# Performance work log

Measured on AMD Instinct MI355X. Metric: run time of the kernel, lower is better.

Reference implementation:

```python
import jax, jax.numpy as jnp
import numpy as np
import math

DIM = 2048
N_HEADS = 32
N_KV_HEADS = 8
HEAD_DIM = DIM // N_HEADS  # 64
N_REP = N_HEADS // N_KV_HEADS  # 4
BSZ, SEQ = 2, 2048


def setup_inputs() -> dict:
    key = jax.random.key(0)
    ks = jax.random.split(key, 8)
    x = jax.random.normal(ks[0], (BSZ, SEQ, DIM), dtype=jnp.float32)
    # rotary tables, [seq, head_dim//2]
    inv_freq = 1.0 / (10000.0 ** (np.arange(0, HEAD_DIM, 2, dtype=np.float32) / HEAD_DIM))
    t = np.arange(SEQ, dtype=np.float32)
    freqs = np.outer(t, inv_freq)
    freqs_cos = jnp.asarray(np.cos(freqs))
    freqs_sin = jnp.asarray(np.sin(freqs))
    s = 0.02
    wq = jax.random.normal(ks[1], (DIM, N_HEADS * HEAD_DIM), dtype=jnp.float32) * s
    wk = jax.random.normal(ks[2], (DIM, N_KV_HEADS * HEAD_DIM), dtype=jnp.float32) * s
    wv = jax.random.normal(ks[3], (DIM, N_KV_HEADS * HEAD_DIM), dtype=jnp.float32) * s
    wo = jax.random.normal(ks[4], (N_HEADS * HEAD_DIM, DIM), dtype=jnp.float32) * s
    return {"x": x, "freqs_cos": freqs_cos, "freqs_sin": freqs_sin,
            "wq": wq, "wk": wk, "wv": wv, "wo": wo}


def _apply_rotary(xq, xk, cos, sin):
    # xq: [b,s,h,d], xk: [b,s,kh,d]; cos/sin: [s, d//2]
    def rot(t):
        tr = t[..., 0::2]  # even -> real
        ti = t[..., 1::2]  # odd  -> imag
        c = cos[None, :, None, :]
        s_ = sin[None, :, None, :]
        or_ = tr * c - ti * s_
        oi_ = tr * s_ + ti * c
        # interleave back: [..., d//2, 2] -> [..., d]
        return jnp.stack([or_, oi_], axis=-1).reshape(t.shape)
    return rot(xq), rot(xk)


def reference(x, freqs_cos, freqs_sin, wq, wk, wv, wo):
    b, s, _ = x.shape
    xq = (x @ wq).reshape(b, s, N_HEADS, HEAD_DIM)
    xk = (x @ wk).reshape(b, s, N_KV_HEADS, HEAD_DIM)
    xv = (x @ wv).reshape(b, s, N_KV_HEADS, HEAD_DIM)
    xq, xk = _apply_rotary(xq, xk, freqs_cos, freqs_sin)
    # repeat_kv: [b,s,kh,d] -> [b,s,kh*n_rep,d]
    xk = jnp.repeat(xk, N_REP, axis=2)
    xv = jnp.repeat(xv, N_REP, axis=2)
    # [b,h,s,d]
    q = xq.transpose(0, 2, 1, 3)
    k = xk.transpose(0, 2, 1, 3)
    v = xv.transpose(0, 2, 1, 3)
    scale = 1.0 / math.sqrt(HEAD_DIM)
    scores = jnp.einsum('bhqd,bhkd->bhqk', q, k) * scale
    causal = jnp.tril(jnp.ones((s, s), dtype=bool))
    scores = jnp.where(causal[None, None], scores, jnp.float32(-jnp.inf))
    probs = jax.nn.softmax(scores, axis=-1)
    out = jnp.einsum('bhqk,bhkd->bhqd', probs, v)  # [b,h,s,d]
    out = out.transpose(0, 2, 1, 3).reshape(b, s, N_HEADS * HEAD_DIM)
    return out @ wo
```

## Files before the change

### kernel.cpp

```cpp
#include <hip/hip_runtime.h>
#include <hip/hip_bf16.h>

typedef __attribute__((ext_vector_type(8))) short short8;
typedef __attribute__((ext_vector_type(4))) float f32x4;

__device__ __forceinline__ unsigned short f2bf(float f) {
  union { float f; unsigned u; } v; v.f = f;
  unsigned r = v.u + 0x7FFFu + ((v.u >> 16) & 1u);
  return (unsigned short)(r >> 16);
}
__device__ __forceinline__ float bf2f(unsigned short h) {
  union { unsigned u; float f; } v; v.u = ((unsigned)h) << 16;
  return v.f;
}
__device__ __forceinline__ unsigned pkbf(float a, float b) {
  __hip_bfloat162 h = __float22bfloat162_rn(float2{a, b});
  union { __hip_bfloat162 h; unsigned u; } cv; cv.h = h;
  return cv.u;
}

__global__ void prep(const float* __restrict__ x, const float* __restrict__ wq,
                     const float* __restrict__ wk, const float* __restrict__ wv,
                     const float* __restrict__ wo, unsigned short* __restrict__ xb,
                     unsigned short* __restrict__ wt, unsigned short* __restrict__ wot) {
  const int z = blockIdx.z, tid = threadIdx.x;
  if (z == 0) {
    int id = blockIdx.y * 64 + blockIdx.x;
#pragma unroll
    for (int rep = 0; rep < 2; ++rep) {
      int i = (rep * 4096 + id) * 256 + tid;
      float4 v = ((const float4*)x)[i];
      ushort4 o;
      o.x = f2bf(v.x); o.y = f2bf(v.y); o.z = f2bf(v.z); o.w = f2bf(v.w);
      ((ushort4*)xb)[i] = o;
    }
    return;
  }
  __shared__ float tile[32][33];
  const float* src;
  unsigned short* dst;
  int N;
  if (z == 1) { src = wq; dst = wt; N = 2048; }
  else if (z == 2) { src = wk; dst = wt + 2048ull * 2048; N = 512; }
  else if (z == 3) { src = wv; dst = wt + 2560ull * 2048; N = 512; }
  else { src = wo; dst = wot; N = 2048; }
  const int K = 2048;
  int n0 = blockIdx.x * 32, k0 = blockIdx.y * 32;
  if (n0 >= N) return;
  int xx = tid & 31, yy = tid >> 5;
#pragma unroll
  for (int j = 0; j < 4; ++j) tile[yy + 8 * j][xx] = src[(size_t)(k0 + yy + 8 * j) * N + n0 + xx];
  __syncthreads();
#pragma unroll
  for (int j = 0; j < 4; ++j) dst[(size_t)(n0 + yy + 8 * j) * K + k0 + xx] = f2bf(tile[xx][yy + 8 * j]);
}

template <int MODE>
__global__ __launch_bounds__(256, 2) void gemm_bt64(const unsigned short* __restrict__ A,
                                                    const unsigned short* __restrict__ Bt,
                                                    void* __restrict__ Cv, int K, int ldc,
                                                    unsigned short* __restrict__ vt) {
  __shared__ alignas(16) unsigned short As[128 * 64];
  __shared__ alignas(16) unsigned short Bs[128 * 64];
  const int t = threadIdx.x;
  const int lane = t & 63, w = t >> 6;
  const int l15 = lane & 15, quad = lane >> 4;
  const int bn0 = blockIdx.x * 128, bm0 = blockIdx.y * 128;
  const int wm = (w >> 1) * 64, wn = (w & 1) * 64;
  const unsigned short* Ab = A + (size_t)bm0 * K;
  const unsigned short* Bb = Bt + (size_t)bn0 * K;
  const int asw = l15 & 7;

  f32x4 acc[4][4];
  const f32x4 zf = {0.f, 0.f, 0.f, 0.f};
#pragma unroll
  for (int i = 0; i < 4; ++i)
#pragma unroll
    for (int j = 0; j < 4; ++j) acc[i][j] = zf;

  for (int k0 = 0; k0 < K; k0 += 64) {
    __syncthreads();
#pragma unroll
    for (int r = 0; r < 4; ++r) {
      int e = r * 256 + t;
      int row = e >> 3, cslot = e & 7;
      int cg = cslot ^ (row & 7);
      const unsigned short* ga = Ab + (size_t)row * K + k0 + cg * 8;
      __builtin_amdgcn_global_load_lds((const __attribute__((address_space(1))) void*)ga,
                                       (__attribute__((address_space(3))) void*)(As + e * 8), 16, 0, 0);
      const unsigned short* gb = Bb + (size_t)row * K + k0 + cg * 8;
      __builtin_amdgcn_global_load_lds((const __attribute__((address_space(1))) void*)gb,
                                       (__attribute__((address_space(3))) void*)(Bs + e * 8), 16, 0, 0);
    }
    __syncthreads();
#pragma unroll
    for (int s = 0; s < 2; ++s) {
      short8 af[4], bf[4];
#pragma unroll
      for (int i = 0; i < 4; ++i)
        af[i] = *reinterpret_cast<const short8*>(As + (wm + i * 16 + l15) * 64 + (((s * 4 + quad) ^ asw) * 8));
#pragma unroll
      for (int j = 0; j < 4; ++j)
        bf[j] = *reinterpret_cast<const short8*>(Bs + (wn + j * 16 + l15) * 64 + (((s * 4 + quad) ^ asw) * 8));
#pragma unroll
      for (int i = 0; i < 4; ++i)
#pragma unroll
        for (int j = 0; j < 4; ++j)
          acc[i][j] = __builtin_amdgcn_mfma_f32_16x16x32_bf16(af[i], bf[j], acc[i][j], 0, 0, 0);
    }
  }

  if (MODE == 1 && bn0 >= 2560) {
    const int b = bm0 >> 11;
#pragma unroll
    for (int i = 0; i < 4; ++i) {
      int srow = (bm0 + wm + i * 16 + quad * 4) & 2047;
#pragma unroll
      for (int j = 0; j < 4; ++j) {
        int vcol = bn0 - 2560 + wn + j * 16 + l15;
        int kvh = vcol >> 6, d = vcol & 63;
        uint2 pk = make_uint2(pkbf(acc[i][j][0], acc[i][j][1]), pkbf(acc[i][j][2], acc[i][j][3]));
        *reinterpret_cast<uint2*>(vt + ((size_t)(b * 8 + kvh) * 64 + d) * 2048 + srow) = pk;
      }
    }
  } else {
#pragma unroll
    for (int i = 0; i < 4; ++i)
#pragma unroll
      for (int j = 0; j < 4; ++j)
#pragma unroll
        for (int r = 0; r < 4; ++r) {
          size_t row = (size_t)(bm0 + wm + i * 16 + quad * 4 + r);
          size_t col = (size_t)(bn0 + wn + j * 16 + l15);
          if (MODE == 1)
            ((unsigned short*)Cv)[row * ldc + col] = f2bf(acc[i][j][r]);
          else
            ((float*)Cv)[row * ldc + col] = acc[i][j][r];
        }
  }
}

__global__ void rope_k(unsigned short* __restrict__ qkv, const float* __restrict__ fcos,
                       const float* __restrict__ fsin) {
  int tid = blockIdx.x * 256 + threadIdx.x;
  int row = tid >> 8, p = tid & 255;
  int col = 2048 + 2 * p;
  int s = row & 2047;
  int fi = p & 31;
  float c = fcos[s * 32 + fi], sn = fsin[s * 32 + fi];
  unsigned int* ptr = (unsigned int*)(qkv + (size_t)row * 2560 + col);
  unsigned int pr = *ptr;
  float xr = bf2f((unsigned short)(pr & 0xFFFFu));
  float xi = bf2f((unsigned short)(pr >> 16));
  float orr = xr * c - xi * sn;
  float oi = xr * sn + xi * c;
  *ptr = ((unsigned)f2bf(oi) << 16) | (unsigned)f2bf(orr);
}

__global__ __launch_bounds__(256, 4) void flash_attn(const unsigned short* __restrict__ qkv,
                                                     const unsigned short* __restrict__ vt,
                                                     const float* __restrict__ fcos,
                                                     const float* __restrict__ fsin,
                                                     unsigned short* __restrict__ out) {
  __shared__ alignas(16) unsigned short Ks[64 * 64];
  __shared__ alignas(16) unsigned short Vs[64 * 64];
  __shared__ alignas(16) unsigned short Ps[128 * 64];
  __shared__ float Ls[128];
  const int t = threadIdx.x, lane = t & 63, w = t >> 6;
  const int l15 = lane & 15, quad = lane >> 4;
  const int h = blockIdx.y, b = blockIdx.z;
  const int qb = ((int)blockIdx.x ^ (15 * (h >> 4))) & 15;
  const int q0 = qb * 128;
  const int kvh = h >> 2;
  const size_t rowB = (size_t)b * 2048;
  const unsigned short* Qg = qkv + (rowB + q0) * 2560 + h * 64;
  const unsigned short* Kg = qkv + rowB * 2560 + 2048 + kvh * 64;
  const unsigned short* Vtg = vt + (size_t)(b * 8 + kvh) * 64 * 2048;
  const float SC = 0.18033688011112042f;

  short8 qf[2][2];
#pragma unroll
  for (int mt = 0; mt < 2; ++mt)
#pragma unroll
    for (int s = 0; s < 2; ++s) {
      int qrow = w * 32 + mt * 16 + l15;
      short8 raw = *reinterpret_cast<const short8*>(Qg + (size_t)qrow * 2560 + s * 32 + quad * 8);
      f32x4 c4 = *reinterpret_cast<const f32x4*>(fcos + (size_t)(q0 + qrow) * 32 + s * 16 + quad * 4);
      f32x4 s4 = *reinterpret_cast<const f32x4*>(fsin + (size_t)(q0 + qrow) * 32 + s * 16 + quad * 4);
      short8 o;
#pragma unroll
      for (int k = 0; k < 4; ++k) {
        float xr = bf2f((unsigned short)raw[2 * k]);
        float xi = bf2f((unsigned short)raw[2 * k + 1]);
        o[2 * k] = (short)f2bf((xr * c4[k] - xi * s4[k]) * SC);
        o[2 * k + 1] = (short)f2bf((xr * s4[k] + xi * c4[k]) * SC);
      }
      qf[mt][s] = o;
    }

  const f32x4 zf = {0.f, 0.f, 0.f, 0.f};
  f32x4 oacc[2][4];
#pragma unroll
  for (int mt = 0; mt < 2; ++mt)
#pragma unroll
    for (int nt = 0; nt < 4; ++nt) oacc[mt][nt] = zf;
  float lsum[2] = {0.f, 0.f};

  const int kb_end = 2 * qb + 2;
  const int srow = t >> 3, sc8 = t & 7;
  const int soff = srow * 64 + ((sc8 ^ (srow & 7)) * 8);
  const int asw = l15 & 7;
  short8 kreg[2], vreg[2];
#pragma unroll
  for (int r = 0; r < 2; ++r) {
    kreg[r] = *reinterpret_cast<const short8*>(Kg + (size_t)(srow + 32 * r) * 2560 + sc8 * 8);
    vreg[r] = *reinterpret_cast<const short8*>(Vtg + (size_t)(srow + 32 * r) * 2048 + sc8 * 8);
  }

  for (int kb = 0; kb < kb_end; ++kb) {
    __syncthreads();
#pragma unroll
    for (int r = 0; r < 2; ++r) {
      *reinterpret_cast<short8*>(Ks + soff + r * 32 * 64) = kreg[r];
      *reinterpret_cast<short8*>(Vs + soff + r * 32 * 64) = vreg[r];
    }
    __syncthreads();
    if (kb + 1 < kb_end) {
#pragma unroll
      for (int r = 0; r < 2; ++r) {
        kreg[r] = *reinterpret_cast<const short8*>(Kg + (size_t)((kb + 1) * 64 + srow + 32 * r) * 2560 + sc8 * 8);
        vreg[r] = *reinterpret_cast<const short8*>(Vtg + (size_t)(srow + 32 * r) * 2048 + (kb + 1) * 64 + sc8 * 8);
      }
    }
    const int qmaxw = q0 + w * 32 + 31;
    if (kb * 64 > qmaxw) continue;
    const bool needMask = (kb * 64 + 63) > (q0 + w * 32);

#pragma unroll
    for (int kvt = 0; kvt < 4; ++kvt) {
      f32x4 st0 = zf, st1 = zf;
#pragma unroll
      for (int s = 0; s < 2; ++s) {
        short8 kf = *reinterpret_cast<const short8*>(Ks + (kvt * 16 + l15) * 64 + ((s * 4 + quad) ^ asw) * 8);
        st0 = __builtin_amdgcn_mfma_f32_16x16x32_bf16(kf, qf[0][s], st0, 0, 0, 0);
        st1 = __builtin_amdgcn_mfma_f32_16x16x32_bf16(kf, qf[1][s], st1, 0, 0, 0);
      }
      const int pcol = ((kvt * 2 + (quad >> 1)) ^ asw) * 8 + (quad & 1) * 4;
      if (needMask) {
        const int kvb = kb * 64 + kvt * 16 + quad * 4;
#pragma unroll
        for (int qt = 0; qt < 2; ++qt) {
          const f32x4 stv = qt ? st1 : st0;
          const int qg = q0 + w * 32 + qt * 16 + l15;
          float p[4];
#pragma unroll
          for (int r = 0; r < 4; ++r) {
            float pv = __builtin_amdgcn_exp2f(stv[r]);
            p[r] = (kvb + r > qg) ? 0.f : pv;
          }
          lsum[qt] += (p[0] + p[1]) + (p[2] + p[3]);
          *reinterpret_cast<uint2*>(Ps + (size_t)(w * 32 + qt * 16 + l15) * 64 + pcol) =
              make_uint2(pkbf(p[0], p[1]), pkbf(p[2], p[3]));
        }
      } else {
#pragma unroll
        for (int qt = 0; qt < 2; ++qt) {
          const f32x4 stv = qt ? st1 : st0;
          float p[4];
#pragma unroll
          for (int r = 0; r < 4; ++r) p[r] = __builtin_amdgcn_exp2f(stv[r]);
          lsum[qt] += (p[0] + p[1]) + (p[2] + p[3]);
          *reinterpret_cast<uint2*>(Ps + (size_t)(w * 32 + qt * 16 + l15) * 64 + pcol) =
              make_uint2(pkbf(p[0], p[1]), pkbf(p[2], p[3]));
        }
      }
    }

#pragma unroll
    for (int s = 0; s < 2; ++s) {
      short8 vf[4];
#pragma unroll
      for (int nt = 0; nt < 4; ++nt)
        vf[nt] = *reinterpret_cast<const short8*>(Vs + (nt * 16 + l15) * 64 + ((s * 4 + quad) ^ asw) * 8);
#pragma unroll
      for (int mt = 0; mt < 2; ++mt) {
        short8 pf = *reinterpret_cast<const short8*>(Ps + (size_t)(w * 32 + mt * 16 + l15) * 64 + ((s * 4 + quad) ^ asw) * 8);
#pragma unroll
        for (int nt = 0; nt < 4; ++nt)
          oacc[mt][nt] = __builtin_amdgcn_mfma_f32_16x16x32_bf16(pf, vf[nt], oacc[mt][nt], 0, 0, 0);
      }
    }
  }

#pragma unroll
  for (int qt = 0; qt < 2; ++qt) {
    lsum[qt] += __shfl_xor(lsum[qt], 16, 64);
    lsum[qt] += __shfl_xor(lsum[qt], 32, 64);
  }
  if (quad == 0) {
    Ls[w * 32 + l15] = lsum[0];
    Ls[w * 32 + 16 + l15] = lsum[1];
  }
  float linv[2][4];
#pragma unroll
  for (int mt = 0; mt < 2; ++mt)
#pragma unroll
    for (int r = 0; r < 4; ++r) linv[mt][r] = 1.f / Ls[w * 32 + mt * 16 + quad * 4 + r];

#pragma unroll
  for (int mt = 0; mt < 2; ++mt)
#pragma unroll
    for (int nt = 0; nt < 4; ++nt)
#pragma unroll
      for (int r = 0; r < 4; ++r) {
        size_t row = rowB + (size_t)(q0 + w * 32 + mt * 16 + quad * 4 + r);
        size_t col = (size_t)h * 64 + nt * 16 + l15;
        out[row * 2048 + col] = f2bf(oacc[mt][nt][r] * linv[mt][r]);
      }
}

extern "C" void kernel_launch(void* const* d_in, const int* in_sizes, int n_in, void* d_out,
                              int out_size, void* d_ws, size_t ws_size, hipStream_t stream) {
  const float* x = (const float*)d_in[0];
  const float* fcos = (const float*)d_in[1];
  const float* fsin = (const float*)d_in[2];
  const float* wq = (const float*)d_in[3];
  const float* wk = (const float*)d_in[4];
  const float* wv = (const float*)d_in[5];
  const float* wo = (const float*)d_in[6];

  char* ws = (char*)d_ws;
  unsigned short* xb = (unsigned short*)ws;
  unsigned short* wt = (unsigned short*)(ws + 16777216ull);
  unsigned short* wot = (unsigned short*)(ws + 29360128ull);
  unsigned short* qkv = (unsigned short*)(ws + 37748736ull);
  unsigned short* attno = (unsigned short*)(ws + 58720256ull);
  unsigned short* vt = (unsigned short*)(ws + 75497472ull);

  prep<<<dim3(64, 64, 5), 256, 0, stream>>>(x, wq, wk, wv, wo, xb, wt, wot);
  gemm_bt64<1><<<dim3(24, 32), 256, 0, stream>>>(xb, wt, qkv, 2048, 2560, vt);
  rope_k<<<4096, 256, 0, stream>>>(qkv, fcos, fsin);
  flash_attn<<<dim3(16, 32, 2), 256, 0, stream>>>(qkv, vt, fcos, fsin, attno);
  gemm_bt64<0><<<dim3(16, 32), 256, 0, stream>>>(attno, wot, d_out, 2048, 2048, nullptr);
}
```

Measured before the change: 272.0 us.

## Fuse K rope into QKV GEMM epilogue and use atomic work queue for attention

Removes the standalone rope kernel by applying rotary embedding to K columns in the QKV GEMM epilogue, using a lane shuffle to fetch each element's pair partner. Flash attention now handles 256-row query tiles with 64 rows per wave. Blocks pull work items from a global atomic counter in heaviest-first order, so causal work is balanced dynamically. The kernel also skips fully masked key subtiles. The counter is stored in the output buffer and zeroed with a memset, and the output GEMM later overwrites it. The larger tiles double shared memory and registers and halve occupancy.

```diff
diff --git a/kernel.cpp b/kernel.cpp
--- a/kernel.cpp
+++ b/kernel.cpp
@@ -59,7 +59,9 @@
 __global__ __launch_bounds__(256, 2) void gemm_bt64(const unsigned short* __restrict__ A,
                                                     const unsigned short* __restrict__ Bt,
                                                     void* __restrict__ Cv, int K, int ldc,
-                                                    unsigned short* __restrict__ vt) {
+                                                    unsigned short* __restrict__ vt,
+                                                    const float* __restrict__ fcos,
+                                                    const float* __restrict__ fsin) {
   __shared__ alignas(16) unsigned short As[128 * 64];
   __shared__ alignas(16) unsigned short Bs[128 * 64];
   const int t = threadIdx.x;
@@ -123,6 +125,26 @@
         *reinterpret_cast<uint2*>(vt + ((size_t)(b * 8 + kvh) * 64 + d) * 2048 + srow) = pk;
       }
     }
+  } else if (MODE == 1 && bn0 >= 2048) {
+#pragma unroll
+    for (int i = 0; i < 4; ++i) {
+      int row = bm0 + wm + i * 16 + quad * 4;
+      int s0 = row & 2047;
+#pragma unroll
+      for (int j = 0; j < 4; ++j) {
+        int col = bn0 + wn + j * 16 + l15;
+        int f = (col & 63) >> 1;
+        float sign = (col & 1) ? 1.f : -1.f;
+#pragma unroll
+        for (int r = 0; r < 4; ++r) {
+          float v = acc[i][j][r];
+          float partner = __shfl_xor(v, 1, 64);
+          float c = fcos[(size_t)(s0 + r) * 32 + f];
+          float sn = fsin[(size_t)(s0 + r) * 32 + f];
+          ((unsigned short*)Cv)[(size_t)(row + r) * ldc + col] = f2bf(v * c + sign * partner * sn);
+        }
+      }
+    }
   } else {
 #pragma unroll
     for (int i = 0; i < 4; ++i)
@@ -140,183 +162,186 @@
   }
 }
 
-__global__ void rope_k(unsigned short* __restrict__ qkv, const float* __restrict__ fcos,
-                       const float* __restrict__ fsin) {
-  int tid = blockIdx.x * 256 + threadIdx.x;
-  int row = tid >> 8, p = tid & 255;
-  int col = 2048 + 2 * p;
-  int s = row & 2047;
-  int fi = p & 31;
-  float c = fcos[s * 32 + fi], sn = fsin[s * 32 + fi];
-  unsigned int* ptr = (unsigned int*)(qkv + (size_t)row * 2560 + col);
-  unsigned int pr = *ptr;
-  float xr = bf2f((unsigned short)(pr & 0xFFFFu));
-  float xi = bf2f((unsigned short)(pr >> 16));
-  float orr = xr * c - xi * sn;
-  float oi = xr * sn + xi * c;
-  *ptr = ((unsigned)f2bf(oi) << 16) | (unsigned)f2bf(orr);
-}
-
-__global__ __launch_bounds__(256, 4) void flash_attn(const unsigned short* __restrict__ qkv,
+__global__ __launch_bounds__(256, 2) void flash_attn(const unsigned short* __restrict__ qkv,
                                                      const unsigned short* __restrict__ vt,
                                                      const float* __restrict__ fcos,
                                                      const float* __restrict__ fsin,
-                                                     unsigned short* __restrict__ out) {
+                                                     unsigned short* __restrict__ out,
+                                                     int* __restrict__ cnt) {
   __shared__ alignas(16) unsigned short Ks[64 * 64];
   __shared__ alignas(16) unsigned short Vs[64 * 64];
-  __shared__ alignas(16) unsigned short Ps[128 * 64];
-  __shared__ float Ls[128];
+  __shared__ alignas(16) unsigned short Ps[256 * 64];
+  __shared__ float Ls[256];
+  __shared__ int s_item;
   const int t = threadIdx.x, lane = t & 63, w = t >> 6;
   const int l15 = lane & 15, quad = lane >> 4;
-  const int h = blockIdx.y, b = blockIdx.z;
-  const int qb = ((int)blockIdx.x ^ (15 * (h >> 4))) & 15;
-  const int q0 = qb * 128;
-  const int kvh = h >> 2;
-  const size_t rowB = (size_t)b * 2048;
-  const unsigned short* Qg = qkv + (rowB + q0) * 2560 + h * 64;
-  const unsigned short* Kg = qkv + rowB * 2560 + 2048 + kvh * 64;
-  const unsigned short* Vtg = vt + (size_t)(b * 8 + kvh) * 64 * 2048;
-  const float SC = 0.18033688011112042f;
-
-  short8 qf[2][2];
-#pragma unroll
-  for (int mt = 0; mt < 2; ++mt)
-#pragma unroll
-    for (int s = 0; s < 2; ++s) {
-      int qrow = w * 32 + mt * 16 + l15;
-      short8 raw = *reinterpret_cast<const short8*>(Qg + (size_t)qrow * 2560 + s * 32 + quad * 8);
-      f32x4 c4 = *reinterpret_cast<const f32x4*>(fcos + (size_t)(q0 + qrow) * 32 + s * 16 + quad * 4);
-      f32x4 s4 = *reinterpret_cast<const f32x4*>(fsin + (size_t)(q0 + qrow) * 32 + s * 16 + quad * 4);
-      short8 o;
-#pragma unroll
-      for (int k = 0; k < 4; ++k) {
-        float xr = bf2f((unsigned short)raw[2 * k]);
-        float xi = bf2f((unsigned short)raw[2 * k + 1]);
-        o[2 * k] = (short)f2bf((xr * c4[k] - xi * s4[k]) * SC);
-        o[2 * k + 1] = (short)f2bf((xr * s4[k] + xi * c4[k]) * SC);
-      }
-      qf[mt][s] = o;
-    }
-
-  const f32x4 zf = {0.f, 0.f, 0.f, 0.f};
-  f32x4 oacc[2][4];
-#pragma unroll
-  for (int mt = 0; mt < 2; ++mt)
-#pragma unroll
-    for (int nt = 0; nt < 4; ++nt) oacc[mt][nt] = zf;
-  float lsum[2] = {0.f, 0.f};
-
-  const int kb_end = 2 * qb + 2;
   const int srow = t >> 3, sc8 = t & 7;
   const int soff = srow * 64 + ((sc8 ^ (srow & 7)) * 8);
   const int asw = l15 & 7;
-  short8 kreg[2], vreg[2];
-#pragma unroll
-  for (int r = 0; r < 2; ++r) {
-    kreg[r] = *reinterpret_cast<const short8*>(Kg + (size_t)(srow + 32 * r) * 2560 + sc8 * 8);
-    vreg[r] = *reinterpret_cast<const short8*>(Vtg + (size_t)(srow + 32 * r) * 2048 + sc8 * 8);
+  const float SC = 0.18033688011112042f;
+  const f32x4 zf = {0.f, 0.f, 0.f, 0.f};
+
+  while (true) {
+    __syncthreads();
+    if (t == 0) s_item = atomicAdd(cnt, 1);
+    __syncthreads();
+    const int item = s_item;
+    if (item >= 512) break;
+    const int qb = 7 - (item >> 6);
+    const int rest = item & 63;
+    const int h = rest & 31, b = rest >> 5;
+    const int q0 = qb * 256;
+    const int kvh = h >> 2;
+    const size_t rowB = (size_t)b * 2048;
+    const unsigned short* Qg = qkv + (rowB + q0) * 2560 + h * 64;
+    const unsigned short* Kg = qkv + rowB * 2560 + 2048 + kvh * 64;
+    const unsigned short* Vtg = vt + (size_t)(b * 8 + kvh) * 64 * 2048;
+
+    short8 qf[4][2];
+#pragma unroll
+    for (int mt = 0; mt < 4; ++mt)
+#pragma unroll
+      for (int s = 0; s < 2; ++s) {
+        int qrow = w * 64 + mt * 16 + l15;
+        short8 raw = *reinterpret_cast<const short8*>(Qg + (size_t)qrow * 2560 + s * 32 + quad * 8);
+        f32x4 c4 = *reinterpret_cast<const f32x4*>(fcos + (size_t)(q0 + qrow) * 32 + s * 16 + quad * 4);
+        f32x4 s4 = *reinterpret_cast<const f32x4*>(fsin + (size_t)(q0 + qrow) * 32 + s * 16 + quad * 4);
+        short8 o;
+#pragma unroll
+        for (int k = 0; k < 4; ++k) {
+          float xr = bf2f((unsigned short)raw[2 * k]);
+          float xi = bf2f((unsigned short)raw[2 * k + 1]);
+          o[2 * k] = (short)f2bf((xr * c4[k] - xi * s4[k]) * SC);
+          o[2 * k + 1] = (short)f2bf((xr * s4[k] + xi * c4[k]) * SC);
+        }
+        qf[mt][s] = o;
+      }
+
+    f32x4 oacc[4][4];
+#pragma unroll
+    for (int mt = 0; mt < 4; ++mt)
+#pragma unroll
+      for (int nt = 0; nt < 4; ++nt) oacc[mt][nt] = zf;
+    float lsum[4] = {0.f, 0.f, 0.f, 0.f};
+
+    const int kb_end = 4 * (qb + 1);
+    const int qmaxw = q0 + w * 64 + 63;
+    short8 kreg[2], vreg[2];
+#pragma unroll
+    for (int r = 0; r < 2; ++r) {
+      kreg[r] = *reinterpret_cast<const short8*>(Kg + (size_t)(srow + 32 * r) * 2560 + sc8 * 8);
+      vreg[r] = *reinterpret_cast<const short8*>(Vtg + (size_t)(srow + 32 * r) * 2048 + sc8 * 8);
+    }
+
+    for (int kb = 0; kb < kb_end; ++kb) {
+      __syncthreads();
+#pragma unroll
+      for (int r = 0; r < 2; ++r) {
+        *reinterpret_cast<short8*>(Ks + soff + r * 32 * 64) = kreg[r];
+        *reinterpret_cast<short8*>(Vs + soff + r * 32 * 64) = vreg[r];
+      }
+      __syncthreads();
+      if (kb + 1 < kb_end) {
+#pragma unroll
+        for (int r = 0; r < 2; ++r) {
+          kreg[r] = *reinterpret_cast<const short8*>(Kg + (size_t)((kb + 1) * 64 + srow + 32 * r) * 2560 + sc8 * 8);
+          vreg[r] = *reinterpret_cast<const short8*>(Vtg + (size_t)(srow + 32 * r) * 2048 + (kb + 1) * 64 + sc8 * 8);
+        }
+      }
+      if (kb * 64 > qmaxw) continue;
+      const bool needMask = (kb * 64 + 63) > (q0 + w * 64);
+
+#pragma unroll
+      for (int kvt = 0; kvt < 4; ++kvt) {
+        if (needMask && (kb * 64 + (kvt >> 1) * 32 > qmaxw)) continue;
+        const int pcol = ((kvt * 2 + (quad >> 1)) ^ asw) * 8 + (quad & 1) * 4;
+        if (needMask && (kb * 64 + kvt * 16 > qmaxw)) {
+#pragma unroll
+          for (int mt = 0; mt < 4; ++mt)
+            *reinterpret_cast<uint2*>(Ps + (size_t)(w * 64 + mt * 16 + l15) * 64 + pcol) = make_uint2(0u, 0u);
+          continue;
+        }
+        f32x4 st[4];
+#pragma unroll
+        for (int mt = 0; mt < 4; ++mt) st[mt] = zf;
+#pragma unroll
+        for (int s = 0; s < 2; ++s) {
+          short8 kf = *reinterpret_cast<const short8*>(Ks + (kvt * 16 + l15) * 64 + ((s * 4 + quad) ^ asw) * 8);
+#pragma unroll
+          for (int mt = 0; mt < 4; ++mt)
+            st[mt] = __builtin_amdgcn_mfma_f32_16x16x32_bf16(kf, qf[mt][s], st[mt], 0, 0, 0);
+        }
+        if (needMask) {
+          const int kvb = kb * 64 + kvt * 16 + quad * 4;
+#pragma unroll
+          for (int mt = 0; mt < 4; ++mt) {
+            const int qg = q0 + w * 64 + mt * 16 + l15;
+            float p[4];
+#pragma unroll
+            for (int r = 0; r < 4; ++r) {
+              float pv = __builtin_amdgcn_exp2f(st[mt][r]);
+              p[r] = (kvb + r > qg) ? 0.f : pv;
+            }
+            lsum[mt] += (p[0] + p[1]) + (p[2] + p[3]);
+            *reinterpret_cast<uint2*>(Ps + (size_t)(w * 64 + mt * 16 + l15) * 64 + pcol) =
+                make_uint2(pkbf(p[0], p[1]), pkbf(p[2], p[3]));
+          }
+        } else {
+#pragma unroll
+          for (int mt = 0; mt < 4; ++mt) {
+            float p[4];
+#pragma unroll
+            for (int r = 0; r < 4; ++r) p[r] = __builtin_amdgcn_exp2f(st[mt][r]);
+            lsum[mt] += (p[0] + p[1]) + (p[2] + p[3]);
+            *reinterpret_cast<uint2*>(Ps + (size_t)(w * 64 + mt * 16 + l15) * 64 + pcol) =
+                make_uint2(pkbf(p[0], p[1]), pkbf(p[2], p[3]));
+          }
+        }
+      }
+
+#pragma unroll
+      for (int s = 0; s < 2; ++s) {
+        if (needMask && (kb * 64 + s * 32 > qmaxw)) continue;
+        short8 vf[4];
+#pragma unroll
+        for (int nt = 0; nt < 4; ++nt)
+          vf[nt] = *reinterpret_cast<const short8*>(Vs + (nt * 16 + l15) * 64 + ((s * 4 + quad) ^ asw) * 8);
+#pragma unroll
+        for (int mt = 0; mt < 4; ++mt) {
+          short8 pf = *reinterpret_cast<const short8*>(Ps + (size_t)(w * 64 + mt * 16 + l15) * 64 + ((s * 4 + quad) ^ asw) * 8);
+#pragma unroll
+          for (int nt = 0; nt < 4; ++nt)
+            oacc[mt][nt] = __builtin_amdgcn_mfma_f32_16x16x32_bf16(pf, vf[nt], oacc[mt][nt], 0, 0, 0);
+        }
+      }
+    }
+
+#pragma unroll
+    for (int mt = 0; mt < 4; ++mt) {
+      lsum[mt] += __shfl_xor(lsum[mt], 16, 64);
+      lsum[mt] += __shfl_xor(lsum[mt], 32, 64);
+    }
+    if (quad == 0) {
+#pragma unroll
+      for (int mt = 0; mt < 4; ++mt) Ls[w * 64 + mt * 16 + l15] = lsum[mt];
+    }
+    float linv[4][4];
+#pragma unroll
+    for (int mt = 0; mt < 4; ++mt)
+#pragma unroll
+      for (int r = 0; r < 4; ++r) linv[mt][r] = 1.f / Ls[w * 64 + mt * 16 + quad * 4 + r];
+
+#pragma unroll
+    for (int mt = 0; mt < 4; ++mt)
+#pragma unroll
+      for (int nt = 0; nt < 4; ++nt)
+#pragma unroll
+        for (int r = 0; r < 4; ++r) {
+          size_t row = rowB + (size_t)(q0 + w * 64 + mt * 16 + quad * 4 + r);
+          size_t col = (size_t)h * 64 + nt * 16 + l15;
+          out[row * 2048 + col] = f2bf(oacc[mt][nt][r] * linv[mt][r]);
+        }
   }
-
-  for (int kb = 0; kb < kb_end; ++kb) {
-    __syncthreads();
-#pragma unroll
-    for (int r = 0; r < 2; ++r) {
-      *reinterpret_cast<short8*>(Ks + soff + r * 32 * 64) = kreg[r];
-      *reinterpret_cast<short8*>(Vs + soff + r * 32 * 64) = vreg[r];
-    }
-    __syncthreads();
-    if (kb + 1 < kb_end) {
-#pragma unroll
-      for (int r = 0; r < 2; ++r) {
-        kreg[r] = *reinterpret_cast<const short8*>(Kg + (size_t)((kb + 1) * 64 + srow + 32 * r) * 2560 + sc8 * 8);
-        vreg[r] = *reinterpret_cast<const short8*>(Vtg + (size_t)(srow + 32 * r) * 2048 + (kb + 1) * 64 + sc8 * 8);
-      }
-    }
-    const int qmaxw = q0 + w * 32 + 31;
-    if (kb * 64 > qmaxw) continue;
-    const bool needMask = (kb * 64 + 63) > (q0 + w * 32);
-
-#pragma unroll
-    for (int kvt = 0; kvt < 4; ++kvt) {
-      f32x4 st0 = zf, st1 = zf;
-#pragma unroll
-      for (int s = 0; s < 2; ++s) {
-        short8 kf = *reinterpret_cast<const short8*>(Ks + (kvt * 16 + l15) * 64 + ((s * 4 + quad) ^ asw) * 8);
-        st0 = __builtin_amdgcn_mfma_f32_16x16x32_bf16(kf, qf[0][s], st0, 0, 0, 0);
-        st1 = __builtin_amdgcn_mfma_f32_16x16x32_bf16(kf, qf[1][s], st1, 0, 0, 0);
-      }
-      const int pcol = ((kvt * 2 + (quad >> 1)) ^ asw) * 8 + (quad & 1) * 4;
-      if (needMask) {
-        const int kvb = kb * 64 + kvt * 16 + quad * 4;
-#pragma unroll
-        for (int qt = 0; qt < 2; ++qt) {
-          const f32x4 stv = qt ? st1 : st0;
-          const int qg = q0 + w * 32 + qt * 16 + l15;
-          float p[4];
-#pragma unroll
-          for (int r = 0; r < 4; ++r) {
-            float pv = __builtin_amdgcn_exp2f(stv[r]);
-            p[r] = (kvb + r > qg) ? 0.f : pv;
-          }
-          lsum[qt] += (p[0] + p[1]) + (p[2] + p[3]);
-          *reinterpret_cast<uint2*>(Ps + (size_t)(w * 32 + qt * 16 + l15) * 64 + pcol) =
-              make_uint2(pkbf(p[0], p[1]), pkbf(p[2], p[3]));
-        }
-      } else {
-#pragma unroll
-        for (int qt = 0; qt < 2; ++qt) {
-          const f32x4 stv = qt ? st1 : st0;
-          float p[4];
-#pragma unroll
-          for (int r = 0; r < 4; ++r) p[r] = __builtin_amdgcn_exp2f(stv[r]);
-          lsum[qt] += (p[0] + p[1]) + (p[2] + p[3]);
-          *reinterpret_cast<uint2*>(Ps + (size_t)(w * 32 + qt * 16 + l15) * 64 + pcol) =
-              make_uint2(pkbf(p[0], p[1]), pkbf(p[2], p[3]));
-        }
-      }
-    }
-
-#pragma unroll
-    for (int s = 0; s < 2; ++s) {
-      short8 vf[4];
-#pragma unroll
-      for (int nt = 0; nt < 4; ++nt)
-        vf[nt] = *reinterpret_cast<const short8*>(Vs + (nt * 16 + l15) * 64 + ((s * 4 + quad) ^ asw) * 8);
-#pragma unroll
-      for (int mt = 0; mt < 2; ++mt) {
-        short8 pf = *reinterpret_cast<const short8*>(Ps + (size_t)(w * 32 + mt * 16 + l15) * 64 + ((s * 4 + quad) ^ asw) * 8);
-#pragma unroll
-        for (int nt = 0; nt < 4; ++nt)
-          oacc[mt][nt] = __builtin_amdgcn_mfma_f32_16x16x32_bf16(pf, vf[nt], oacc[mt][nt], 0, 0, 0);
-      }
-    }
-  }
-
-#pragma unroll
-  for (int qt = 0; qt < 2; ++qt) {
-    lsum[qt] += __shfl_xor(lsum[qt], 16, 64);
-    lsum[qt] += __shfl_xor(lsum[qt], 32, 64);
-  }
-  if (quad == 0) {
-    Ls[w * 32 + l15] = lsum[0];
-    Ls[w * 32 + 16 + l15] = lsum[1];
-  }
-  float linv[2][4];
-#pragma unroll
-  for (int mt = 0; mt < 2; ++mt)
-#pragma unroll
-    for (int r = 0; r < 4; ++r) linv[mt][r] = 1.f / Ls[w * 32 + mt * 16 + quad * 4 + r];
-
-#pragma unroll
-  for (int mt = 0; mt < 2; ++mt)
-#pragma unroll
-    for (int nt = 0; nt < 4; ++nt)
-#pragma unroll
-      for (int r = 0; r < 4; ++r) {
-        size_t row = rowB + (size_t)(q0 + w * 32 + mt * 16 + quad * 4 + r);
-        size_t col = (size_t)h * 64 + nt * 16 + l15;
-        out[row * 2048 + col] = f2bf(oacc[mt][nt][r] * linv[mt][r]);
-      }
 }
 
 extern "C" void kernel_launch(void* const* d_in, const int* in_sizes, int n_in, void* d_out,
@@ -336,10 +361,11 @@
   unsigned short* qkv = (unsigned short*)(ws + 37748736ull);
   unsigned short* attno = (unsigned short*)(ws + 58720256ull);
   unsigned short* vt = (unsigned short*)(ws + 75497472ull);
-
+  int* cnt = (int*)d_out;
+
+  hipMemsetAsync(cnt, 0, 4, stream);
   prep<<<dim3(64, 64, 5), 256, 0, stream>>>(x, wq, wk, wv, wo, xb, wt, wot);
-  gemm_bt64<1><<<dim3(24, 32), 256, 0, stream>>>(xb, wt, qkv, 2048, 2560, vt);
-  rope_k<<<4096, 256, 0, stream>>>(qkv, fcos, fsin);
-  flash_attn<<<dim3(16, 32, 2), 256, 0, stream>>>(qkv, vt, fcos, fsin, attno);
-  gemm_bt64<0><<<dim3(16, 32), 256, 0, stream>>>(attno, wot, d_out, 2048, 2048, nullptr);
-}
+  gemm_bt64<1><<<dim3(24, 32), 256, 0, stream>>>(xb, wt, qkv, 2048, 2560, vt, fcos, fsin);
+  flash_attn<<<512, 256, 0, stream>>>(qkv, vt, fcos, fsin, attno, cnt);
+  gemm_bt64<0><<<dim3(16, 32), 256, 0, stream>>>(attno, wot, d_out, 2048, 2048, nullptr, nullptr, nullptr);
+}
```

New measurement: 317.8 us. 16.8% more time.
